# Kernel tuning notes

Measured on AMD Instinct MI355X. Metric: run time of the kernel, lower is better.

## Reference

```python
import jax, jax.numpy as jnp
import numpy as np

# ---- fixed 22-node graph from the module's build_graph (clique expansion of adj_list) ----
_ADJ_LIST = [[0, 2, 5, 8, 11], [0, 1, 4, 7, 10], [0, 3, 6, 9, 12, 15],
             [9, 14, 17, 19, 21], [9, 13, 16, 18, 20]]
_N = max(max(s) for s in _ADJ_LIST) + 1  # 22
_A = np.zeros((_N, _N), dtype=np.float32)
for s in _ADJ_LIST:
    for i in range(len(s)):
        for j in range(i + 1, len(s)):
            _A[s[i], s[j]] = 1.0
            _A[s[j], s[i]] = 1.0
_deg = _A.sum(axis=1)
_dinv = 1.0 / np.sqrt(np.maximum(_deg, 1.0))
A_HAT = jnp.asarray(_dinv[:, None] * _A * _dinv[None, :])  # D^{-1/2} A D^{-1/2}, DGL norm='both'

SEQ_LEN = 100
HID = 3


def setup_inputs() -> dict:
    key = jax.random.key(0)
    ks = jax.random.split(key, 9)
    B, IN = 16384, 32
    s_in = 1.0 / np.sqrt(IN)
    s_h = 1.0 / np.sqrt(HID)
    return {
        "x": jax.random.normal(ks[0], (B, IN), jnp.float32),
        "w_r_W": jax.random.normal(ks[1], (IN, HID), jnp.float32) * s_in,
        "w_r_b": jax.random.normal(ks[2], (HID,), jnp.float32) * s_in,
        "w_z_W": jax.random.normal(ks[3], (IN, HID), jnp.float32) * s_in,
        "w_z_b": jax.random.normal(ks[4], (HID,), jnp.float32) * s_in,
        "w_h_W": jax.random.normal(ks[5], (IN, HID), jnp.float32) * s_in,
        "w_h_b": jax.random.normal(ks[6], (HID,), jnp.float32) * s_in,
        "gcn_W": jax.random.normal(ks[7], (HID, HID), jnp.float32) * s_h,
        "gcn_b": jax.random.normal(ks[8], (HID,), jnp.float32) * s_h,
    }


def reference(x, w_r_W, w_r_b, w_z_W, w_z_b, w_h_W, w_h_b, gcn_W, gcn_b):
    B = x.shape[0]
    # input projections are constant across timesteps and nodes -> compute once, broadcast
    xr = (x @ w_r_W + w_r_b)[:, None, :]  # (B,1,H)
    xz = (x @ w_z_W + w_z_b)[:, None, :]
    xh = (x @ w_h_W + w_h_b)[:, None, :]

    def step(h, _):
        # GraphConv: symmetric-normalized aggregation, then linear + bias
        gh = jnp.einsum('nm,bmh->bnh', A_HAT, h) @ gcn_W + gcn_b  # (B,N,H)
        r = jax.nn.sigmoid(xr + gh)
        z = jax.nn.sigmoid(xz + gh)
        h_tilde = jnp.tanh(xh + r * gh)
        h_new = (1.0 - z) * h + z * h_tilde
        return h_new, h_new

    h0 = jnp.zeros((B, _N, HID), x.dtype)
    _, hs = jax.lax.scan(step, h0, None, length=SEQ_LEN)  # (T,B,N,H)
    out = jnp.transpose(hs, (1, 0, 2, 3)).reshape(B, -1)  # (B, T*N*H)
    return out
```

## Files before the change

kernel.cpp:

```cpp
#include <hip/hip_runtime.h>


#define TPB1 64
#define GRID1 (16384 / TPB1)
#define T_TOTAL 100
#define SCH 10
#define NCHUNK (T_TOTAL / SCH)
#define REC 12
#define ROWF (T_TOTAL * REC)
#define ROWF4 (ROWF / 4)
#define CH_F4 (SCH * REC / 4)
#define K1_ITERS 30

#define TPB2 256
#define BPB2 16
#define GRID2 (16384 / BPB2)
#define OUT_ROW_F4 1650
#define OUT_ELEMS 6600

#define FREP 4
#define FRPW 16
#define FGRID (16384 / TPB1 * FREP)
#define FROW_F4 (SCH * 66 / 4)
#define FSTRIDE (SCH * 9 + 1)
#define FSTG (TPB1 * FSTRIDE)
#define F4_PER_REP (FRPW * FROW_F4)
#define FGITERS ((F4_PER_REP + TPB1 - 1) / TPB1)

#if __has_builtin(__builtin_amdgcn_exp2f)
#define EXP2F __builtin_amdgcn_exp2f
#else
#define EXP2F exp2f
#endif
#if __has_builtin(__builtin_amdgcn_rcpf)
#define RCPF __builtin_amdgcn_rcpf
#else
#define RCPF(x) (1.0f / (x))
#endif

static __device__ __forceinline__ float fast_sigmoid(float x) {
    float e = EXP2F(-1.44269504f * x);
    return RCPF(1.0f + e);
}
static __device__ __forceinline__ float fast_tanh(float x) {
    float e = EXP2F(2.88539008f * x);
    return 1.0f - 2.0f * RCPF(1.0f + e);
}

__device__ const unsigned char d_cls3[66] = {
    0,1,2, 3,4,5, 3,4,5, 6,7,8, 3,4,5, 3,4,5, 6,7,8, 3,4,5, 3,4,5,
    0,1,2, 3,4,5, 3,4,5, 6,7,8, 3,4,5, 3,4,5, 6,7,8, 3,4,5, 3,4,5,
    3,4,5, 3,4,5, 3,4,5, 3,4,5
};

struct GruConsts {
    float xr[3], xz[3], xh[3];
    float W9[9], gb3[3];
};

static __device__ __forceinline__ void load_consts_and_project(
    const float* __restrict__ x, int b,
    const float* __restrict__ wS,
    const float* __restrict__ gwS, const float* __restrict__ gbS,
    GruConsts& C)
{
    float xv[32];
    const float4* xp = reinterpret_cast<const float4*>(x + (size_t)b * 32);
    #pragma unroll
    for (int i = 0; i < 8; ++i) {
        float4 v = xp[i];
        xv[4*i+0] = v.x; xv[4*i+1] = v.y; xv[4*i+2] = v.z; xv[4*i+3] = v.w;
    }
    #pragma unroll
    for (int j = 0; j < 3; ++j) { C.xr[j] = wS[288+j]; C.xz[j] = wS[291+j]; C.xh[j] = wS[294+j]; }
    #pragma unroll
    for (int i = 0; i < 32; ++i) {
        float xi = xv[i];
        #pragma unroll
        for (int j = 0; j < 3; ++j) {
            C.xr[j] = fmaf(xi, wS[i*3+j],       C.xr[j]);
            C.xz[j] = fmaf(xi, wS[96 + i*3+j],  C.xz[j]);
            C.xh[j] = fmaf(xi, wS[192 + i*3+j], C.xh[j]);
        }
    }
    #pragma unroll
    for (int i = 0; i < 9; ++i) C.W9[i] = gwS[i];
    #pragma unroll
    for (int j = 0; j < 3; ++j) C.gb3[j] = gbS[j];
}

static __device__ __forceinline__ void gru_step(float* __restrict__ h, const GruConsts& C)
{
    const float M00 = 0.0769230769f;
    const float M01 = 1.1094003925f;
    const float M02 = 0.4961389384f;
    const float M10 = 0.1386750491f;
    const float M11 = 0.75f;
    const float M20 = 0.2480694691f;
    const float M22 = 0.6f;

    float mh[9], gh[9];
    #pragma unroll
    for (int j = 0; j < 3; ++j) {
        mh[j]     = M00 * h[j] + M01 * h[3+j] + M02 * h[6+j];
        mh[3 + j] = M10 * h[j] + M11 * h[3+j];
        mh[6 + j] = M20 * h[j] + M22 * h[6+j];
    }
    #pragma unroll
    for (int c = 0; c < 3; ++c)
        #pragma unroll
        for (int j = 0; j < 3; ++j)
            gh[c*3+j] = C.gb3[j] + mh[c*3+0]*C.W9[j] + mh[c*3+1]*C.W9[3+j] + mh[c*3+2]*C.W9[6+j];
    #pragma unroll
    for (int c = 0; c < 3; ++c) {
        #pragma unroll
        for (int j = 0; j < 3; ++j) {
            float g  = gh[c*3+j];
            float r  = fast_sigmoid(C.xr[j] + g);
            float z  = fast_sigmoid(C.xz[j] + g);
            float ht = fast_tanh(C.xh[j] + r * g);
            float hv = h[c*3+j];
            h[c*3+j] = hv + z * (ht - hv);
        }
    }
}

static __device__ __forceinline__ void stage_weights(
    int tid, int stride,
    const float* __restrict__ w_r_W, const float* __restrict__ w_r_b,
    const float* __restrict__ w_z_W, const float* __restrict__ w_z_b,
    const float* __restrict__ w_h_W, const float* __restrict__ w_h_b,
    const float* __restrict__ gcn_W, const float* __restrict__ gcn_b,
    float* __restrict__ wS, float* __restrict__ gwS, float* __restrict__ gbS)
{
    for (int i = tid; i < 96; i += stride) {
        wS[i]       = w_r_W[i];
        wS[96 + i]  = w_z_W[i];
        wS[192 + i] = w_h_W[i];
    }
    if (tid < 3) {
        wS[288 + tid] = w_r_b[tid];
        wS[291 + tid] = w_z_b[tid];
        wS[294 + tid] = w_h_b[tid];
        gbS[tid] = gcn_b[tid];
    }
    if (tid < 9) gwS[tid] = gcn_W[tid];
}

__global__ __launch_bounds__(TPB1) void gcgru_compute(
    const float* __restrict__ x,
    const float* __restrict__ w_r_W, const float* __restrict__ w_r_b,
    const float* __restrict__ w_z_W, const float* __restrict__ w_z_b,
    const float* __restrict__ w_h_W, const float* __restrict__ w_h_b,
    const float* __restrict__ gcn_W, const float* __restrict__ gcn_b,
    float* __restrict__ compact)
{
    __shared__ float wS[297];
    __shared__ float gwS[9];
    __shared__ float gbS[3];
    __shared__ float stage[TPB1 * SCH * REC];

    const int tid = threadIdx.x;
    const int b0  = blockIdx.x * TPB1;

    stage_weights(tid, TPB1, w_r_W, w_r_b, w_z_W, w_z_b, w_h_W, w_h_b,
                  gcn_W, gcn_b, wS, gwS, gbS);

    GruConsts C;
    load_consts_and_project(x, b0 + tid, wS, gwS, gbS, C);

    float h[9];
    #pragma unroll
    for (int i = 0; i < 9; ++i) h[i] = 0.0f;

    float4* cmp4 = reinterpret_cast<float4*>(compact);

    for (int chunk = 0; chunk < NCHUNK; ++chunk) {
        float* stw = stage + tid * (SCH * REC);

        #pragma unroll
        for (int s = 0; s < SCH; ++s) {
            gru_step(h, C);
            #pragma unroll
            for (int q = 0; q < 9; ++q) stw[s*REC + q] = h[q];
            stw[s*REC + 9] = 0.0f; stw[s*REC + 10] = 0.0f; stw[s*REC + 11] = 0.0f;
        }

        const int cbase = chunk * CH_F4;
        #pragma unroll
        for (int i = 0; i < K1_ITERS; ++i) {
            int f  = i * TPB1 + tid;
            int rl = f / CH_F4;
            int j4 = f - rl * CH_F4;
            const float4* srow = reinterpret_cast<const float4*>(stage + rl * (SCH * REC));
            cmp4[(size_t)(b0 + rl) * ROWF4 + cbase + j4] = srow[j4];
        }
    }
}

__global__ __launch_bounds__(TPB2) void gcgru_expand(
    const float* __restrict__ compact,
    float* __restrict__ out)
{
    __shared__ unsigned short tabE[OUT_ELEMS];

    const int tid = threadIdx.x;
    const int b0  = blockIdx.x * BPB2;

    for (int jj = tid; jj < OUT_ELEMS; jj += TPB2) {
        int t = jj / 66;
        int k = jj - 66 * t;
        tabE[jj] = (unsigned short)(t * REC + d_cls3[k]);
    }
    __syncthreads();

    float4* out4 = reinterpret_cast<float4*>(out);

    for (int r = 0; r < BPB2; ++r) {
        const float* cp = compact + (size_t)(b0 + r) * ROWF;
        float4* orow = out4 + (size_t)(b0 + r) * OUT_ROW_F4;
        for (int j4 = tid; j4 < OUT_ROW_F4; j4 += TPB2) {
            int jj = 4 * j4;
            float4 v;
            v.x = cp[tabE[jj + 0]];
            v.y = cp[tabE[jj + 1]];
            v.z = cp[tabE[jj + 2]];
            v.w = cp[tabE[jj + 3]];
            orow[j4] = v;
        }
    }
}

__global__ __launch_bounds__(TPB1) void gcgru_fused(
    const float* __restrict__ x,
    const float* __restrict__ w_r_W, const float* __restrict__ w_r_b,
    const float* __restrict__ w_z_W, const float* __restrict__ w_z_b,
    const float* __restrict__ w_h_W, const float* __restrict__ w_h_b,
    const float* __restrict__ gcn_W, const float* __restrict__ gcn_b,
    float* __restrict__ out)
{
    __shared__ float wS[297];
    __shared__ float gwS[9];
    __shared__ float gbS[3];
    __shared__ unsigned int tabS[FROW_F4];
    __shared__ float stage[FSTG];

    const int tid = threadIdx.x;
    const int rep = blockIdx.x & (FREP - 1);
    const int b0  = (blockIdx.x >> 2) * TPB1;
    const int row0 = rep * FRPW;

    stage_weights(tid, TPB1, w_r_W, w_r_b, w_z_W, w_z_b, w_h_W, w_h_b,
                  gcn_W, gcn_b, wS, gwS, gbS);
    for (int j4 = tid; j4 < FROW_F4; j4 += TPB1) {
        unsigned int w = 0;
        #pragma unroll
        for (int u = 0; u < 4; ++u) {
            int jj = 4 * j4 + u;
            int tl = jj / 66;
            int k  = jj - 66 * tl;
            w |= (unsigned int)(tl * 9 + d_cls3[k]) << (8 * u);
        }
        tabS[j4] = w;
    }

    GruConsts C;
    load_consts_and_project(x, b0 + tid, wS, gwS, gbS, C);

    float h[9];
    #pragma unroll
    for (int i = 0; i < 9; ++i) h[i] = 0.0f;

    float4* out4 = reinterpret_cast<float4*>(out);

    for (int chunk = 0; chunk < NCHUNK; ++chunk) {
        float* stw = stage + tid * FSTRIDE;
        #pragma unroll
        for (int s = 0; s < SCH; ++s) {
            gru_step(h, C);
            #pragma unroll
            for (int q = 0; q < 9; ++q) stw[s*9 + q] = h[q];
        }
        const int cbase = chunk * FROW_F4;
        for (int i = 0; i < FGITERS; ++i) {
            int f = i * TPB1 + tid;
            if (f < F4_PER_REP) {
                int rl = f / FROW_F4;
                int j4 = f - rl * FROW_F4;
                int r  = row0 + rl;
                unsigned int tw = tabS[j4];
                const float* row = stage + r * FSTRIDE;
                float4 v;
                v.x = row[tw & 255u];
                v.y = row[(tw >> 8)  & 255u];
                v.z = row[(tw >> 16) & 255u];
                v.w = row[tw >> 24];
                out4[(size_t)(b0 + r) * OUT_ROW_F4 + cbase + j4] = v;
            }
        }
    }
}

extern "C" void kernel_launch(void* const* d_in, const int* in_sizes, int n_in,
                              void* d_out, int out_size, void* d_ws, size_t ws_size,
                              hipStream_t stream) {
    const float* xp     = (const float*)d_in[0];
    const float* w_r_W  = (const float*)d_in[1];
    const float* w_r_b  = (const float*)d_in[2];
    const float* w_z_W  = (const float*)d_in[3];
    const float* w_z_b  = (const float*)d_in[4];
    const float* w_h_W  = (const float*)d_in[5];
    const float* w_h_b  = (const float*)d_in[6];
    const float* gcn_W  = (const float*)d_in[7];
    const float* gcn_b  = (const float*)d_in[8];
    float* outp = (float*)d_out;

    const size_t need = (size_t)16384 * ROWF * sizeof(float);
    if (ws_size >= need && d_ws != nullptr) {
        float* compact = (float*)d_ws;
        gcgru_compute<<<GRID1, TPB1, 0, stream>>>(xp, w_r_W, w_r_b, w_z_W, w_z_b,
                                                  w_h_W, w_h_b, gcn_W, gcn_b, compact);
        gcgru_expand<<<GRID2, TPB2, 0, stream>>>(compact, outp);
    } else {
        gcgru_fused<<<FGRID, TPB1, 0, stream>>>(xp, w_r_W, w_r_b, w_z_W, w_z_b,
                                                w_h_W, w_h_b, gcn_W, gcn_b, outp);
    }
}
```

Before: 581.1 us.

## Store compact GRU states time-major and flatten expand kernel into grid sweep

```diff
diff --git a/kernel.cpp b/kernel.cpp
--- a/kernel.cpp
+++ b/kernel.cpp
@@ -1,28 +1,29 @@
 #include <hip/hip_runtime.h>
 
 
+#define B_TOT 16384
+#define T_TOTAL 100
+#define REC 12
+#define TSLAB (B_TOT * REC)
+#define CMP_FLOATS ((size_t)T_TOTAL * TSLAB)
+
 #define TPB1 64
-#define GRID1 (16384 / TPB1)
-#define T_TOTAL 100
-#define SCH 10
-#define NCHUNK (T_TOTAL / SCH)
-#define REC 12
-#define ROWF (T_TOTAL * REC)
-#define ROWF4 (ROWF / 4)
-#define CH_F4 (SCH * REC / 4)
-#define K1_ITERS 30
+#define GRID1 (B_TOT / TPB1)
 
 #define TPB2 256
-#define BPB2 16
-#define GRID2 (16384 / BPB2)
+#define GRID2 1056
+#define ITERS2 100
+#define SWEEP (GRID2 * TPB2)
 #define OUT_ROW_F4 1650
 #define OUT_ELEMS 6600
 
-#define FREP 4
-#define FRPW 16
-#define FGRID (16384 / TPB1 * FREP)
-#define FROW_F4 (SCH * 66 / 4)
-#define FSTRIDE (SCH * 9 + 1)
+#define FREP 8
+#define FRPW (TPB1 / FREP)
+#define FGRID (B_TOT / TPB1 * FREP)
+#define FSCH 4
+#define FNCHUNK (T_TOTAL / FSCH)
+#define FROW_F4 (FSCH * 66 / 4)
+#define FSTRIDE (FSCH * 9 + 1)
 #define FSTG (TPB1 * FSTRIDE)
 #define F4_PER_REP (FRPW * FROW_F4)
 #define FGITERS ((F4_PER_REP + TPB1 - 1) / TPB1)
@@ -58,10 +59,12 @@
     float W9[9], gb3[3];
 };
 
-static __device__ __forceinline__ void load_consts_and_project(
+static __device__ __forceinline__ void project_inputs(
     const float* __restrict__ x, int b,
     const float* __restrict__ wS,
-    const float* __restrict__ gwS, const float* __restrict__ gbS,
+    const float* __restrict__ w_r_b, const float* __restrict__ w_z_b,
+    const float* __restrict__ w_h_b,
+    const float* __restrict__ gcn_W, const float* __restrict__ gcn_b,
     GruConsts& C)
 {
     float xv[32];
@@ -72,7 +75,7 @@
         xv[4*i+0] = v.x; xv[4*i+1] = v.y; xv[4*i+2] = v.z; xv[4*i+3] = v.w;
     }
     #pragma unroll
-    for (int j = 0; j < 3; ++j) { C.xr[j] = wS[288+j]; C.xz[j] = wS[291+j]; C.xh[j] = wS[294+j]; }
+    for (int j = 0; j < 3; ++j) { C.xr[j] = w_r_b[j]; C.xz[j] = w_z_b[j]; C.xh[j] = w_h_b[j]; }
     #pragma unroll
     for (int i = 0; i < 32; ++i) {
         float xi = xv[i];
@@ -84,9 +87,9 @@
         }
     }
     #pragma unroll
-    for (int i = 0; i < 9; ++i) C.W9[i] = gwS[i];
-    #pragma unroll
-    for (int j = 0; j < 3; ++j) C.gb3[j] = gbS[j];
+    for (int i = 0; i < 9; ++i) C.W9[i] = gcn_W[i];
+    #pragma unroll
+    for (int j = 0; j < 3; ++j) C.gb3[j] = gcn_b[j];
 }
 
 static __device__ __forceinline__ void gru_step(float* __restrict__ h, const GruConsts& C)
@@ -125,28 +128,6 @@
     }
 }
 
-static __device__ __forceinline__ void stage_weights(
-    int tid, int stride,
-    const float* __restrict__ w_r_W, const float* __restrict__ w_r_b,
-    const float* __restrict__ w_z_W, const float* __restrict__ w_z_b,
-    const float* __restrict__ w_h_W, const float* __restrict__ w_h_b,
-    const float* __restrict__ gcn_W, const float* __restrict__ gcn_b,
-    float* __restrict__ wS, float* __restrict__ gwS, float* __restrict__ gbS)
-{
-    for (int i = tid; i < 96; i += stride) {
-        wS[i]       = w_r_W[i];
-        wS[96 + i]  = w_z_W[i];
-        wS[192 + i] = w_h_W[i];
-    }
-    if (tid < 3) {
-        wS[288 + tid] = w_r_b[tid];
-        wS[291 + tid] = w_z_b[tid];
-        wS[294 + tid] = w_h_b[tid];
-        gbS[tid] = gcn_b[tid];
-    }
-    if (tid < 9) gwS[tid] = gcn_W[tid];
-}
-
 __global__ __launch_bounds__(TPB1) void gcgru_compute(
     const float* __restrict__ x,
     const float* __restrict__ w_r_W, const float* __restrict__ w_r_b,
@@ -155,46 +136,32 @@
     const float* __restrict__ gcn_W, const float* __restrict__ gcn_b,
     float* __restrict__ compact)
 {
-    __shared__ float wS[297];
-    __shared__ float gwS[9];
-    __shared__ float gbS[3];
-    __shared__ float stage[TPB1 * SCH * REC];
+    __shared__ float wS[288];
 
     const int tid = threadIdx.x;
-    const int b0  = blockIdx.x * TPB1;
-
-    stage_weights(tid, TPB1, w_r_W, w_r_b, w_z_W, w_z_b, w_h_W, w_h_b,
-                  gcn_W, gcn_b, wS, gwS, gbS);
+    const int b   = blockIdx.x * TPB1 + tid;
+
+    for (int i = tid; i < 96; i += TPB1) {
+        wS[i]       = w_r_W[i];
+        wS[96 + i]  = w_z_W[i];
+        wS[192 + i] = w_h_W[i];
+    }
 
     GruConsts C;
-    load_consts_and_project(x, b0 + tid, wS, gwS, gbS, C);
+    project_inputs(x, b, wS, w_r_b, w_z_b, w_h_b, gcn_W, gcn_b, C);
 
     float h[9];
     #pragma unroll
     for (int i = 0; i < 9; ++i) h[i] = 0.0f;
 
-    float4* cmp4 = reinterpret_cast<float4*>(compact);
-
-    for (int chunk = 0; chunk < NCHUNK; ++chunk) {
-        float* stw = stage + tid * (SCH * REC);
-
-        #pragma unroll
-        for (int s = 0; s < SCH; ++s) {
-            gru_step(h, C);
-            #pragma unroll
-            for (int q = 0; q < 9; ++q) stw[s*REC + q] = h[q];
-            stw[s*REC + 9] = 0.0f; stw[s*REC + 10] = 0.0f; stw[s*REC + 11] = 0.0f;
-        }
-
-        const int cbase = chunk * CH_F4;
-        #pragma unroll
-        for (int i = 0; i < K1_ITERS; ++i) {
-            int f  = i * TPB1 + tid;
-            int rl = f / CH_F4;
-            int j4 = f - rl * CH_F4;
-            const float4* srow = reinterpret_cast<const float4*>(stage + rl * (SCH * REC));
-            cmp4[(size_t)(b0 + rl) * ROWF4 + cbase + j4] = srow[j4];
-        }
+    for (int t = 0; t < T_TOTAL; ++t) {
+        gru_step(h, C);
+        size_t off = (size_t)t * TSLAB + (size_t)b * REC;
+        float4 v0 = make_float4(h[0], h[1], h[2], h[3]);
+        float4 v1 = make_float4(h[4], h[5], h[6], h[7]);
+        *reinterpret_cast<float4*>(compact + off)     = v0;
+        *reinterpret_cast<float4*>(compact + off + 4) = v1;
+        compact[off + 8] = h[8];
     }
 }
 
@@ -205,29 +172,34 @@
     __shared__ unsigned short tabE[OUT_ELEMS];
 
     const int tid = threadIdx.x;
-    const int b0  = blockIdx.x * BPB2;
-
     for (int jj = tid; jj < OUT_ELEMS; jj += TPB2) {
         int t = jj / 66;
         int k = jj - 66 * t;
-        tabE[jj] = (unsigned short)(t * REC + d_cls3[k]);
+        tabE[jj] = (unsigned short)((t << 4) | d_cls3[k]);
     }
     __syncthreads();
 
     float4* out4 = reinterpret_cast<float4*>(out);
-
-    for (int r = 0; r < BPB2; ++r) {
-        const float* cp = compact + (size_t)(b0 + r) * ROWF;
-        float4* orow = out4 + (size_t)(b0 + r) * OUT_ROW_F4;
-        for (int j4 = tid; j4 < OUT_ROW_F4; j4 += TPB2) {
-            int jj = 4 * j4;
-            float4 v;
-            v.x = cp[tabE[jj + 0]];
-            v.y = cp[tabE[jj + 1]];
-            v.z = cp[tabE[jj + 2]];
-            v.w = cp[tabE[jj + 3]];
-            orow[j4] = v;
-        }
+    const unsigned base = blockIdx.x * TPB2 + tid;
+
+    for (int it = 0; it < ITERS2; ++it) {
+        unsigned idx = (unsigned)it * SWEEP + base;
+        unsigned b   = idx / 1650u;
+        unsigned j4  = idx - b * 1650u;
+        unsigned jj  = j4 * 4u;
+
+        unsigned e0 = tabE[jj + 0];
+        unsigned e1 = tabE[jj + 1];
+        unsigned e2 = tabE[jj + 2];
+        unsigned e3 = tabE[jj + 3];
+
+        const float* cb = compact + (size_t)b * REC;
+        float4 v;
+        v.x = cb[(size_t)(e0 >> 4) * TSLAB + (e0 & 15u)];
+        v.y = cb[(size_t)(e1 >> 4) * TSLAB + (e1 & 15u)];
+        v.z = cb[(size_t)(e2 >> 4) * TSLAB + (e2 & 15u)];
+        v.w = cb[(size_t)(e3 >> 4) * TSLAB + (e3 & 15u)];
+        out4[idx] = v;
     }
 }
 
@@ -239,19 +211,19 @@
     const float* __restrict__ gcn_W, const float* __restrict__ gcn_b,
     float* __restrict__ out)
 {
-    __shared__ float wS[297];
-    __shared__ float gwS[9];
-    __shared__ float gbS[3];
+    __shared__ float stage[FSTG];
     __shared__ unsigned int tabS[FROW_F4];
-    __shared__ float stage[FSTG];
-
-    const int tid = threadIdx.x;
-    const int rep = blockIdx.x & (FREP - 1);
-    const int b0  = (blockIdx.x >> 2) * TPB1;
+
+    const int tid  = threadIdx.x;
+    const int rep  = blockIdx.x & (FREP - 1);
+    const int b0   = (blockIdx.x >> 3) * TPB1;
     const int row0 = rep * FRPW;
 
-    stage_weights(tid, TPB1, w_r_W, w_r_b, w_z_W, w_z_b, w_h_W, w_h_b,
-                  gcn_W, gcn_b, wS, gwS, gbS);
+    for (int i = tid; i < 96; i += TPB1) {
+        stage[i]       = w_r_W[i];
+        stage[96 + i]  = w_z_W[i];
+        stage[192 + i] = w_h_W[i];
+    }
     for (int j4 = tid; j4 < FROW_F4; j4 += TPB1) {
         unsigned int w = 0;
         #pragma unroll
@@ -265,7 +237,7 @@
     }
 
     GruConsts C;
-    load_consts_and_project(x, b0 + tid, wS, gwS, gbS, C);
+    project_inputs(x, b0 + tid, stage, w_r_b, w_z_b, w_h_b, gcn_W, gcn_b, C);
 
     float h[9];
     #pragma unroll
@@ -273,29 +245,36 @@
 
     float4* out4 = reinterpret_cast<float4*>(out);
 
-    for (int chunk = 0; chunk < NCHUNK; ++chunk) {
+    for (int chunk = 0; chunk < FNCHUNK; ++chunk) {
         float* stw = stage + tid * FSTRIDE;
         #pragma unroll
-        for (int s = 0; s < SCH; ++s) {
+        for (int s = 0; s < FSCH; ++s) {
             gru_step(h, C);
             #pragma unroll
             for (int q = 0; q < 9; ++q) stw[s*9 + q] = h[q];
         }
         const int cbase = chunk * FROW_F4;
+        float4 vv[FGITERS];
+        #pragma unroll
+        for (int i = 0; i < FGITERS; ++i) {
+            int f  = i * TPB1 + tid;
+            int fi = (f < F4_PER_REP) ? f : 0;
+            int rl = fi / FROW_F4;
+            int j4 = fi - rl * FROW_F4;
+            unsigned int tw = tabS[j4];
+            const float* row = stage + (row0 + rl) * FSTRIDE;
+            vv[i].x = row[tw & 255u];
+            vv[i].y = row[(tw >> 8)  & 255u];
+            vv[i].z = row[(tw >> 16) & 255u];
+            vv[i].w = row[tw >> 24];
+        }
+        #pragma unroll
         for (int i = 0; i < FGITERS; ++i) {
             int f = i * TPB1 + tid;
             if (f < F4_PER_REP) {
                 int rl = f / FROW_F4;
                 int j4 = f - rl * FROW_F4;
-                int r  = row0 + rl;
-                unsigned int tw = tabS[j4];
-                const float* row = stage + r * FSTRIDE;
-                float4 v;
-                v.x = row[tw & 255u];
-                v.y = row[(tw >> 8)  & 255u];
-                v.z = row[(tw >> 16) & 255u];
-                v.w = row[tw >> 24];
-                out4[(size_t)(b0 + r) * OUT_ROW_F4 + cbase + j4] = v;
+                out4[(size_t)(b0 + row0 + rl) * OUT_ROW_F4 + cbase + j4] = vv[i];
             }
         }
     }
@@ -315,7 +294,7 @@
     const float* gcn_b  = (const float*)d_in[8];
     float* outp = (float*)d_out;
 
-    const size_t need = (size_t)16384 * ROWF * sizeof(float);
+    const size_t need = CMP_FLOATS * sizeof(float);
     if (ws_size >= need && d_ws != nullptr) {
         float* compact = (float*)d_ws;
         gcgru_compute<<<GRID1, TPB1, 0, stream>>>(xp, w_r_W, w_r_b, w_z_W, w_z_b,
```

Measured after the change: 567.5 us. 2.3% less time.
